# Kernel optimization log

Hardware: AMD Instinct MI355X
Metric: run time of the kernel (lower is better)

The kernel has to match this reference:

```python
import jax, jax.numpy as jnp
import numpy as np

D_MODEL, D_K, D_V, N_HEADS = 1024, 64, 64, 16
B, S = 4, 4096
LN_EPS = 1e-5
NORM_EPS = 1e-12  # torch F.normalize default eps


def setup_inputs() -> dict:
    key = jax.random.key(0)
    ks = jax.random.split(key, 9)
    s = 0.02
    return {
        "x": jax.random.normal(ks[0], (B, S, D_MODEL), dtype=jnp.float32),
        # nn.Linear weights have shape [out, in]
        "W_Q": jax.random.normal(ks[1], (N_HEADS * D_K, D_MODEL), dtype=jnp.float32) * s,
        "W_K": jax.random.normal(ks[2], (N_HEADS * D_K, D_MODEL), dtype=jnp.float32) * s,
        "W_V": jax.random.normal(ks[3], (N_HEADS * D_V, D_MODEL), dtype=jnp.float32) * s,
        "W_g": jax.random.normal(ks[4], (N_HEADS * D_V, D_MODEL), dtype=jnp.float32) * s,
        "W_alpha": jax.random.normal(ks[5], (N_HEADS, D_MODEL), dtype=jnp.float32) * s,
        "W_O": jax.random.normal(ks[6], (D_MODEL, N_HEADS * D_V), dtype=jnp.float32) * s,
        "ln_gamma": jnp.ones((D_MODEL,), dtype=jnp.float32),
        "ln_beta": jnp.zeros((D_MODEL,), dtype=jnp.float32),
    }


def reference(x, W_Q, W_K, W_V, W_g, W_alpha, W_O, ln_gamma, ln_beta):
    # --- input projection chain (unfused variant) ---
    Q_raw = jnp.einsum('bsd,od->bso', x, W_Q)               # [B,S,H*Dk] (unused downstream)
    K_raw = jnp.einsum('bsd,od->bso', x, W_K)               # [B,S,H*Dk]
    V = jnp.einsum('bsd,od->bso', x, W_V)                   # [B,S,H*Dv]
    g_raw = jnp.einsum('bsd,od->bso', x, W_g)               # [B,S,H*Dv]
    alpha_raw = jnp.einsum('bsd,od->bso', x, W_alpha)       # [B,S,H]

    # F.normalize over the full last dim (n_heads*d_k), eps clamp on the norm
    K_norm = K_raw / jnp.maximum(jnp.linalg.norm(K_raw, axis=-1, keepdims=True), NORM_EPS)
    gate = jax.nn.silu(g_raw)
    alpha = jax.nn.sigmoid(alpha_raw)

    # scan is simulated as identity: scan_output = V
    scan_output = V

    # --- output epilogue: gate-multiply + output GEMM + residual + LayerNorm ---
    gated = scan_output * gate
    projected = jnp.einsum('bsv,dv->bsd', gated, W_O)
    pre = projected + x
    mean = jnp.mean(pre, axis=-1, keepdims=True)
    var = jnp.mean(jnp.square(pre - mean), axis=-1, keepdims=True)
    out = (pre - mean) * jax.lax.rsqrt(var + LN_EPS) * ln_gamma + ln_beta
    return out
```

## Files before the change

### kernel.cpp

```cpp
#include <hip/hip_runtime.h>

#define M_TOT 16384
#define DM    1024
#define KTILES 32

typedef unsigned short ushort_t;
typedef __bf16 bf16x8 __attribute__((ext_vector_type(8)));
typedef float  f32x4  __attribute__((ext_vector_type(4)));

__device__ __forceinline__ ushort_t f32_to_bf16(float f) {
    union { float f; unsigned u; } v; v.f = f;
    unsigned u = v.u;
    return (ushort_t)((u + 0x7fffu + ((u >> 16) & 1u)) >> 16);
}
__device__ __forceinline__ float bf16_to_f32(ushort_t h) {
    union { unsigned u; float f; } v; v.u = ((unsigned)h) << 16;
    return v.f;
}

__device__ __forceinline__ int sw_off(int c) {
    return ((c >> 2) << 5) + ((((c & 3) ^ ((c >> 3) & 3))) << 3);
}

__global__ __launch_bounds__(256) void cvt_all(const float* __restrict__ x,
                                               const float* __restrict__ wv,
                                               const float* __restrict__ wg,
                                               const float* __restrict__ wo,
                                               ushort_t* __restrict__ xb,
                                               ushort_t* __restrict__ wvb,
                                               ushort_t* __restrict__ wgb,
                                               ushort_t* __restrict__ wob) {
    const long NX = (long)M_TOT * DM / 4, NW = (long)DM * DM / 4;
    long i = (long)blockIdx.x * 256 + threadIdx.x;
    const float* src; ushort_t* dst; long off;
    if (i < NX)               { src = x;  dst = xb;  off = i; }
    else if (i < NX + NW)     { src = wv; dst = wvb; off = i - NX; }
    else if (i < NX + 2 * NW) { src = wg; dst = wgb; off = i - NX - NW; }
    else                      { src = wo; dst = wob; off = i - NX - 2 * NW; }
    const float4 v = ((const float4*)src)[off];
    ushort4 o;
    o.x = f32_to_bf16(v.x); o.y = f32_to_bf16(v.y);
    o.z = f32_to_bf16(v.z); o.w = f32_to_bf16(v.w);
    ((ushort4*)dst)[off] = o;
}

__global__ __launch_bounds__(256, 3) void gemm_vg(
    const ushort_t* __restrict__ A,
    const ushort_t* __restrict__ Wv,
    const ushort_t* __restrict__ Wg,
    ushort_t* __restrict__ gated)
{
    __shared__ __align__(16) ushort_t As[2 * 4096];
    __shared__ __align__(16) ushort_t Bvs[2 * 2048];
    __shared__ __align__(16) ushort_t Bgs[2 * 2048];

    const int flat = blockIdx.x;
    const int g   = flat & 7;
    const int t   = flat >> 3;
    const int n0  = (t & 15) * 64;
    const int m0  = (((t >> 4) << 3) | g) * 128;

    const int tid  = threadIdx.x;
    const int wave = tid >> 6;
    const int lane = tid & 63;

    f32x4 accv[4][2], accg[4][2];
    const f32x4 vzero = {0.f, 0.f, 0.f, 0.f};
#pragma unroll
    for (int i = 0; i < 4; ++i)
#pragma unroll
        for (int j = 0; j < 2; ++j) { accv[i][j] = vzero; accg[i][j] = vzero; }

    const int cA0 = wave * 128 + lane, cA1 = cA0 + 64;
    const int cB  = wave * 64 + lane;
    const long gA0 = (long)(m0 + (cA0 >> 2)) * DM + ((cA0 & 3) << 3);
    const long gA1 = (long)(m0 + (cA1 >> 2)) * DM + ((cA1 & 3) << 3);
    const long gB  = (long)(n0 + (cB  >> 2)) * DM + ((cB  & 3) << 3);
    const int wA0 = sw_off(cA0), wA1 = sw_off(cA1), wB = sw_off(cB);

    const int fr   = lane & 15;
    const int quad = lane >> 4;
    const int sw   = ((quad ^ ((fr >> 1) & 3)) << 3);
    const int wmBase = (wave >> 1) * 64;
    const int wnBase = (wave & 1) * 32;
    int rdA[4], rdB[2];
#pragma unroll
    for (int i = 0; i < 4; ++i) rdA[i] = (wmBase + i * 16 + fr) * 32 + sw;
#pragma unroll
    for (int j = 0; j < 2; ++j) rdB[j] = (wnBase + j * 16 + fr) * 32 + sw;

    auto compute = [&](const ushort_t* pa, const ushort_t* pv, const ushort_t* pg) {
        bf16x8 af[4];
#pragma unroll
        for (int i = 0; i < 4; ++i) af[i] = *(const bf16x8*)(pa + rdA[i]);
#pragma unroll
        for (int j = 0; j < 2; ++j) {
            bf16x8 bv = *(const bf16x8*)(pv + rdB[j]);
            bf16x8 bg = *(const bf16x8*)(pg + rdB[j]);
#pragma unroll
            for (int i = 0; i < 4; ++i) {
                accv[i][j] = __builtin_amdgcn_mfma_f32_16x16x32_bf16(af[i], bv, accv[i][j], 0, 0, 0);
                accg[i][j] = __builtin_amdgcn_mfma_f32_16x16x32_bf16(af[i], bg, accg[i][j], 0, 0, 0);
            }
        }
    };

    int4 rA0 = *(const int4*)(A + gA0);
    int4 rA1 = *(const int4*)(A + gA1);
    int4 rV  = *(const int4*)(Wv + gB);
    int4 rG  = *(const int4*)(Wg + gB);
    unsigned xa = 0, xb = 0;
    *(int4*)(As + xa + wA0)  = rA0;
    *(int4*)(As + xa + wA1)  = rA1;
    *(int4*)(Bvs + xb + wB)  = rV;
    *(int4*)(Bgs + xb + wB)  = rG;
    __syncthreads();

    for (int kt = 0; kt < KTILES - 1; ++kt) {
        const int k0 = (kt + 1) * 32;
        rA0 = *(const int4*)(A + gA0 + k0);
        rA1 = *(const int4*)(A + gA1 + k0);
        rV  = *(const int4*)(Wv + gB + k0);
        rG  = *(const int4*)(Wg + gB + k0);
        compute(As + xa, Bvs + xb, Bgs + xb);
        xa ^= 4096; xb ^= 2048;
        *(int4*)(As + xa + wA0)  = rA0;
        *(int4*)(As + xa + wA1)  = rA1;
        *(int4*)(Bvs + xb + wB)  = rV;
        *(int4*)(Bgs + xb + wB)  = rG;
        __syncthreads();
    }
    compute(As + xa, Bvs + xb, Bgs + xb);

#pragma unroll
    for (int i = 0; i < 4; ++i) {
#pragma unroll
        for (int j = 0; j < 2; ++j) {
            const int colg = n0 + wnBase + j * 16 + fr;
#pragma unroll
            for (int r = 0; r < 4; ++r) {
                const int rowg = m0 + wmBase + i * 16 + quad * 4 + r;
                float v = accv[i][j][r];
                float gg = accg[i][j][r];
                float gate = gg / (1.0f + __expf(-gg));
                gated[rowg * DM + colg] = f32_to_bf16(v * gate);
            }
        }
    }
}

__global__ __launch_bounds__(256, 3) void gemm_o(
    const ushort_t* __restrict__ A,
    const ushort_t* __restrict__ Wo,
    const ushort_t* __restrict__ Xb,
    ushort_t* __restrict__ preout)
{
    __shared__ __align__(16) ushort_t As[2 * 4096];
    __shared__ __align__(16) ushort_t Bs[2 * 4096];

    const int flat = blockIdx.x;
    const int g   = flat & 7;
    const int t   = flat >> 3;
    const int n0  = (t & 7) * 128;
    const int m0  = (((t >> 3) << 3) | g) * 128;

    const int tid  = threadIdx.x;
    const int wave = tid >> 6;
    const int lane = tid & 63;

    f32x4 acc[4][4];
    const f32x4 vzero = {0.f, 0.f, 0.f, 0.f};
#pragma unroll
    for (int i = 0; i < 4; ++i)
#pragma unroll
        for (int j = 0; j < 4; ++j) acc[i][j] = vzero;

    const int cA0 = wave * 128 + lane, cA1 = cA0 + 64;
    const long gA0 = (long)(m0 + (cA0 >> 2)) * DM + ((cA0 & 3) << 3);
    const long gA1 = (long)(m0 + (cA1 >> 2)) * DM + ((cA1 & 3) << 3);
    const long gB0 = (long)(n0 + (cA0 >> 2)) * DM + ((cA0 & 3) << 3);
    const long gB1 = (long)(n0 + (cA1 >> 2)) * DM + ((cA1 & 3) << 3);
    const int wA0 = sw_off(cA0), wA1 = sw_off(cA1);

    const int fr   = lane & 15;
    const int quad = lane >> 4;
    const int sw   = ((quad ^ ((fr >> 1) & 3)) << 3);
    const int wmBase = (wave >> 1) * 64;
    const int wnBase = (wave & 1) * 64;
    int rdA[4], rdB[4];
#pragma unroll
    for (int i = 0; i < 4; ++i) rdA[i] = (wmBase + i * 16 + fr) * 32 + sw;
#pragma unroll
    for (int j = 0; j < 4; ++j) rdB[j] = (wnBase + j * 16 + fr) * 32 + sw;

    auto compute = [&](const ushort_t* pa, const ushort_t* pb) {
        bf16x8 af[4];
#pragma unroll
        for (int i = 0; i < 4; ++i) af[i] = *(const bf16x8*)(pa + rdA[i]);
#pragma unroll
        for (int j = 0; j < 4; ++j) {
            bf16x8 bw = *(const bf16x8*)(pb + rdB[j]);
#pragma unroll
            for (int i = 0; i < 4; ++i)
                acc[i][j] = __builtin_amdgcn_mfma_f32_16x16x32_bf16(af[i], bw, acc[i][j], 0, 0, 0);
        }
    };

    int4 rA0 = *(const int4*)(A + gA0);
    int4 rA1 = *(const int4*)(A + gA1);
    int4 rB0 = *(const int4*)(Wo + gB0);
    int4 rB1 = *(const int4*)(Wo + gB1);
    unsigned xa = 0;
    *(int4*)(As + xa + wA0) = rA0;
    *(int4*)(As + xa + wA1) = rA1;
    *(int4*)(Bs + xa + wA0) = rB0;
    *(int4*)(Bs + xa + wA1) = rB1;
    __syncthreads();

    for (int kt = 0; kt < KTILES - 1; ++kt) {
        const int k0 = (kt + 1) * 32;
        rA0 = *(const int4*)(A + gA0 + k0);
        rA1 = *(const int4*)(A + gA1 + k0);
        rB0 = *(const int4*)(Wo + gB0 + k0);
        rB1 = *(const int4*)(Wo + gB1 + k0);
        compute(As + xa, Bs + xa);
        xa ^= 4096;
        *(int4*)(As + xa + wA0) = rA0;
        *(int4*)(As + xa + wA1) = rA1;
        *(int4*)(Bs + xa + wA0) = rB0;
        *(int4*)(Bs + xa + wA1) = rB1;
        __syncthreads();
    }
    compute(As + xa, Bs + xa);

#pragma unroll
    for (int i = 0; i < 4; ++i) {
#pragma unroll
        for (int j = 0; j < 4; ++j) {
            const int colg = n0 + wnBase + j * 16 + fr;
#pragma unroll
            for (int r = 0; r < 4; ++r) {
                const int rowg = m0 + wmBase + i * 16 + quad * 4 + r;
                float pre = acc[i][j][r] + bf16_to_f32(Xb[rowg * DM + colg]);
                preout[rowg * DM + colg] = f32_to_bf16(pre);
            }
        }
    }
}

__global__ __launch_bounds__(256) void ln_rows(const ushort_t* __restrict__ pre,
                                               const float* __restrict__ gamma,
                                               const float* __restrict__ beta,
                                               float* __restrict__ out)
{
    const int row = blockIdx.x;
    const int tid = threadIdx.x;
    const int wave = tid >> 6, lane = tid & 63;

    ushort4 u = ((const ushort4*)(pre + row * DM))[tid];
    float p0 = bf16_to_f32(u.x), p1 = bf16_to_f32(u.y);
    float p2 = bf16_to_f32(u.z), p3 = bf16_to_f32(u.w);

    float s  = p0 + p1 + p2 + p3;
    float ss = p0 * p0 + p1 * p1 + p2 * p2 + p3 * p3;
#pragma unroll
    for (int off = 32; off > 0; off >>= 1) {
        s  += __shfl_down(s, off);
        ss += __shfl_down(ss, off);
    }
    __shared__ float red[8];
    __shared__ float mb[2];
    if (lane == 0) { red[wave] = s; red[4 + wave] = ss; }
    __syncthreads();
    if (tid == 0) {
        float S  = red[0] + red[1] + red[2] + red[3];
        float SS = red[4] + red[5] + red[6] + red[7];
        float mean = S * (1.0f / 1024.0f);
        float var  = SS * (1.0f / 1024.0f) - mean * mean;
        mb[0] = mean;
        mb[1] = rsqrtf(var + 1e-5f);
    }
    __syncthreads();
    const float mean = mb[0], rs = mb[1];

    float4 gm = ((const float4*)gamma)[tid];
    float4 bt = ((const float4*)beta)[tid];
    float4 o;
    o.x = (p0 - mean) * rs * gm.x + bt.x;
    o.y = (p1 - mean) * rs * gm.y + bt.y;
    o.z = (p2 - mean) * rs * gm.z + bt.z;
    o.w = (p3 - mean) * rs * gm.w + bt.w;
    ((float4*)(out + row * DM))[tid] = o;
}

extern "C" void kernel_launch(void* const* d_in, const int* in_sizes, int n_in,
                              void* d_out, int out_size, void* d_ws, size_t ws_size,
                              hipStream_t stream) {
    const float* x     = (const float*)d_in[0];
    const float* WV    = (const float*)d_in[3];
    const float* WG    = (const float*)d_in[4];
    const float* WO    = (const float*)d_in[6];
    const float* gamma = (const float*)d_in[7];
    const float* beta  = (const float*)d_in[8];
    float* out = (float*)d_out;

    char* ws = (char*)d_ws;
    ushort_t* xb    = (ushort_t*)ws;
    ushort_t* gated = (ushort_t*)(ws + (size_t)M_TOT * DM * 2);
    ushort_t* wvb   = (ushort_t*)(ws + (size_t)M_TOT * DM * 4);
    ushort_t* wgb   = (ushort_t*)(ws + (size_t)M_TOT * DM * 4 + (size_t)DM * DM * 2);
    ushort_t* wob   = (ushort_t*)(ws + (size_t)M_TOT * DM * 4 + (size_t)DM * DM * 4);
    ushort_t* pre   = xb;

    const int nCvt = (M_TOT * DM + 3 * DM * DM) / 4 / 256;
    cvt_all<<<nCvt, 256, 0, stream>>>(x, WV, WG, WO, xb, wvb, wgb, wob);

    gemm_vg<<<2048, 256, 0, stream>>>(xb, wvb, wgb, gated);
    gemm_o <<<1024, 256, 0, stream>>>(gated, wob, xb, pre);
    ln_rows<<<M_TOT, 256, 0, stream>>>(pre, gamma, beta, out);
}
```

Baseline: 284.3 us.

## Replace both GEMMs with 256x256-tile direct-to-LDS pipelined bf16 MFMA kernel

Both bf16 projection GEMMs now use one templated kernel. It has 512 threads and 256x256 output tiles, and loads global memory straight into LDS with global_load_lds, laid out in MFMA fragment order. Loads run through a 4-stage k-pipeline controlled by explicit vmcnt waits and raw barriers, and MFMA issue priority is raised. W_V and W_g are interleaved into one concatenated weight matrix in 16-row groups during conversion, so a single GEMM produces V and gate columns side by side for the SiLU-gate epilogue. The aim is more operand reuse per LDS byte and fewer register-staged copies. The cost is 128KB of dynamic LDS per block, which limits occupancy to one block per CU.

Result: faster. 273.9 us (-3.7%).

```diff
diff --git a/kernel.cpp b/kernel.cpp
--- a/kernel.cpp
+++ b/kernel.cpp
@@ -2,7 +2,6 @@
 
 #define M_TOT 16384
 #define DM    1024
-#define KTILES 32
 
 typedef unsigned short ushort_t;
 typedef __bf16 bf16x8 __attribute__((ext_vector_type(8)));
@@ -18,8 +17,11 @@
     return v.f;
 }
 
-__device__ __forceinline__ int sw_off(int c) {
-    return ((c >> 2) << 5) + ((((c & 3) ^ ((c >> 3) & 3))) << 3);
+__device__ __forceinline__ void gload16(const ushort_t* g, ushort_t* l) {
+    __builtin_amdgcn_global_load_lds(
+        (const __attribute__((address_space(1))) unsigned int*)g,
+        (__attribute__((address_space(3))) unsigned int*)l,
+        16, 0, 0);
 }
 
 __global__ __launch_bounds__(256) void cvt_all(const float* __restrict__ x,
@@ -27,224 +29,147 @@
                                                const float* __restrict__ wg,
                                                const float* __restrict__ wo,
                                                ushort_t* __restrict__ xb,
-                                               ushort_t* __restrict__ wvb,
-                                               ushort_t* __restrict__ wgb,
+                                               ushort_t* __restrict__ wcat,
                                                ushort_t* __restrict__ wob) {
     const long NX = (long)M_TOT * DM / 4, NW = (long)DM * DM / 4;
     long i = (long)blockIdx.x * 256 + threadIdx.x;
-    const float* src; ushort_t* dst; long off;
-    if (i < NX)               { src = x;  dst = xb;  off = i; }
-    else if (i < NX + NW)     { src = wv; dst = wvb; off = i - NX; }
-    else if (i < NX + 2 * NW) { src = wg; dst = wgb; off = i - NX - NW; }
-    else                      { src = wo; dst = wob; off = i - NX - 2 * NW; }
-    const float4 v = ((const float4*)src)[off];
+    const float* src; ushort_t* dst; long so, di;
+    if (i < NX) {
+        src = x; so = i; dst = xb; di = i;
+    } else if (i < NX + NW) {
+        long j = i - NX; src = wv; so = j;
+        int row = (int)(j >> 8), c4 = (int)(j & 255);
+        int orow = ((row >> 4) << 5) | (row & 15);
+        dst = wcat; di = (long)orow * 256 + c4;
+    } else if (i < NX + 2 * NW) {
+        long j = i - NX - 2 * NW + NW;
+        j = i - NX - NW; src = wg; so = j;
+        int row = (int)(j >> 8), c4 = (int)(j & 255);
+        int orow = ((row >> 4) << 5) | 16 | (row & 15);
+        dst = wcat; di = (long)orow * 256 + c4;
+    } else {
+        long j = i - NX - 2 * NW; src = wo; so = j; dst = wob; di = j;
+    }
+    const float4 v = ((const float4*)src)[so];
     ushort4 o;
     o.x = f32_to_bf16(v.x); o.y = f32_to_bf16(v.y);
     o.z = f32_to_bf16(v.z); o.w = f32_to_bf16(v.w);
-    ((ushort4*)dst)[off] = o;
-}
-
-__global__ __launch_bounds__(256, 3) void gemm_vg(
+    ((ushort4*)dst)[di] = o;
+}
+
+template<int EPI>
+__global__ __launch_bounds__(512, 2) void gemm8p(
     const ushort_t* __restrict__ A,
-    const ushort_t* __restrict__ Wv,
-    const ushort_t* __restrict__ Wg,
-    ushort_t* __restrict__ gated)
+    const ushort_t* __restrict__ B,
+    const ushort_t* __restrict__ Xb,
+    ushort_t* __restrict__ out,
+    int nchunk)
 {
-    __shared__ __align__(16) ushort_t As[2 * 4096];
-    __shared__ __align__(16) ushort_t Bvs[2 * 2048];
-    __shared__ __align__(16) ushort_t Bgs[2 * 2048];
+    extern __shared__ ushort_t lds[];
 
     const int flat = blockIdx.x;
-    const int g   = flat & 7;
-    const int t   = flat >> 3;
-    const int n0  = (t & 15) * 64;
-    const int m0  = (((t >> 4) << 3) | g) * 128;
+    const int wgid = (flat & 7) * nchunk + (flat >> 3);
+    const int m0 = (wgid & 63) << 8;
+    const int n0 = (wgid >> 6) << 8;
 
     const int tid  = threadIdx.x;
-    const int wave = tid >> 6;
-    const int lane = tid & 63;
-
-    f32x4 accv[4][2], accg[4][2];
+    const int w    = tid >> 6;
+    const int l    = tid & 63;
+    const int wm   = w >> 2;
+    const int wn   = w & 3;
+    const int fr   = l & 15;
+    const int quad = l >> 4;
+
+    f32x4 acc[8][4];
     const f32x4 vzero = {0.f, 0.f, 0.f, 0.f};
 #pragma unroll
-    for (int i = 0; i < 4; ++i)
-#pragma unroll
-        for (int j = 0; j < 2; ++j) { accv[i][j] = vzero; accg[i][j] = vzero; }
-
-    const int cA0 = wave * 128 + lane, cA1 = cA0 + 64;
-    const int cB  = wave * 64 + lane;
-    const long gA0 = (long)(m0 + (cA0 >> 2)) * DM + ((cA0 & 3) << 3);
-    const long gA1 = (long)(m0 + (cA1 >> 2)) * DM + ((cA1 & 3) << 3);
-    const long gB  = (long)(n0 + (cB  >> 2)) * DM + ((cB  & 3) << 3);
-    const int wA0 = sw_off(cA0), wA1 = sw_off(cA1), wB = sw_off(cB);
-
-    const int fr   = lane & 15;
-    const int quad = lane >> 4;
-    const int sw   = ((quad ^ ((fr >> 1) & 3)) << 3);
-    const int wmBase = (wave >> 1) * 64;
-    const int wnBase = (wave & 1) * 32;
-    int rdA[4], rdB[2];
-#pragma unroll
-    for (int i = 0; i < 4; ++i) rdA[i] = (wmBase + i * 16 + fr) * 32 + sw;
-#pragma unroll
-    for (int j = 0; j < 2; ++j) rdB[j] = (wnBase + j * 16 + fr) * 32 + sw;
-
-    auto compute = [&](const ushort_t* pa, const ushort_t* pv, const ushort_t* pg) {
-        bf16x8 af[4];
-#pragma unroll
-        for (int i = 0; i < 4; ++i) af[i] = *(const bf16x8*)(pa + rdA[i]);
-#pragma unroll
-        for (int j = 0; j < 2; ++j) {
-            bf16x8 bv = *(const bf16x8*)(pv + rdB[j]);
-            bf16x8 bg = *(const bf16x8*)(pg + rdB[j]);
-#pragma unroll
-            for (int i = 0; i < 4; ++i) {
-                accv[i][j] = __builtin_amdgcn_mfma_f32_16x16x32_bf16(af[i], bv, accv[i][j], 0, 0, 0);
-                accg[i][j] = __builtin_amdgcn_mfma_f32_16x16x32_bf16(af[i], bg, accg[i][j], 0, 0, 0);
-            }
+    for (int i = 0; i < 8; ++i)
+#pragma unroll
+        for (int j = 0; j < 4; ++j) acc[i][j] = vzero;
+
+    int srcA[2], srcB[2];
+#pragma unroll
+    for (int h = 0; h < 2; ++h) {
+        srcA[h] = (m0 + h * 128 + w * 16 + fr) * DM + (quad << 3);
+        srcB[h] = (n0 + h * 128 + w * 16 + fr) * DM + (quad << 3);
+    }
+
+    auto stage = [&](int u2) {
+        const int cS   = u2 & 1;
+        const int bufS = (u2 >> 1) & 1;
+        const int koff = (u2 >> 1) * 64 + cS * 32;
+        const int dA   = bufS * 16384 + (cS * 8 + w) * 512;
+#pragma unroll
+        for (int h = 0; h < 2; ++h) {
+            gload16(A + srcA[h] + koff, lds + dA + h * 8192);
+            gload16(B + srcB[h] + koff, lds + 32768 + dA + h * 8192);
         }
     };
 
-    int4 rA0 = *(const int4*)(A + gA0);
-    int4 rA1 = *(const int4*)(A + gA1);
-    int4 rV  = *(const int4*)(Wv + gB);
-    int4 rG  = *(const int4*)(Wg + gB);
-    unsigned xa = 0, xb = 0;
-    *(int4*)(As + xa + wA0)  = rA0;
-    *(int4*)(As + xa + wA1)  = rA1;
-    *(int4*)(Bvs + xb + wB)  = rV;
-    *(int4*)(Bgs + xb + wB)  = rG;
-    __syncthreads();
-
-    for (int kt = 0; kt < KTILES - 1; ++kt) {
-        const int k0 = (kt + 1) * 32;
-        rA0 = *(const int4*)(A + gA0 + k0);
-        rA1 = *(const int4*)(A + gA1 + k0);
-        rV  = *(const int4*)(Wv + gB + k0);
-        rG  = *(const int4*)(Wg + gB + k0);
-        compute(As + xa, Bvs + xb, Bgs + xb);
-        xa ^= 4096; xb ^= 2048;
-        *(int4*)(As + xa + wA0)  = rA0;
-        *(int4*)(As + xa + wA1)  = rA1;
-        *(int4*)(Bvs + xb + wB)  = rV;
-        *(int4*)(Bgs + xb + wB)  = rG;
-        __syncthreads();
-    }
-    compute(As + xa, Bvs + xb, Bgs + xb);
-
-#pragma unroll
-    for (int i = 0; i < 4; ++i) {
-#pragma unroll
-        for (int j = 0; j < 2; ++j) {
-            const int colg = n0 + wnBase + j * 16 + fr;
-#pragma unroll
-            for (int r = 0; r < 4; ++r) {
-                const int rowg = m0 + wmBase + i * 16 + quad * 4 + r;
-                float v = accv[i][j][r];
-                float gg = accg[i][j][r];
-                float gate = gg / (1.0f + __expf(-gg));
-                gated[rowg * DM + colg] = f32_to_bf16(v * gate);
+    stage(0); stage(1);
+
+    for (int u = 0; u < 32; ++u) {
+        if (u < 30) {
+            stage(u + 2);
+            asm volatile("s_waitcnt vmcnt(8)" ::: "memory");
+        } else if (u == 30) {
+            asm volatile("s_waitcnt vmcnt(4)" ::: "memory");
+        } else {
+            asm volatile("s_waitcnt vmcnt(0)" ::: "memory");
+        }
+        __builtin_amdgcn_s_barrier();
+
+        const int buf = (u >> 1) & 1, c = u & 1;
+        const int abase = buf * 16384 + wm * 8192 + c * 4096 + l * 8;
+        const int bbase = 32768 + buf * 16384 + (wn >> 1) * 8192
+                        + (c * 8 + (wn & 1) * 4) * 512 + l * 8;
+        bf16x8 bfrag[4], afrag[8];
+#pragma unroll
+        for (int j = 0; j < 4; ++j) bfrag[j] = *(const bf16x8*)(lds + bbase + j * 512);
+#pragma unroll
+        for (int i = 0; i < 8; ++i) afrag[i] = *(const bf16x8*)(lds + abase + i * 512);
+
+        __builtin_amdgcn_s_setprio(1);
+#pragma unroll
+        for (int j = 0; j < 4; ++j)
+#pragma unroll
+            for (int i = 0; i < 8; ++i)
+                acc[i][j] = __builtin_amdgcn_mfma_f32_16x16x32_bf16(
+                    afrag[i], bfrag[j], acc[i][j], 0, 0, 0);
+        __builtin_amdgcn_s_setprio(0);
+    }
+
+    const int rowb = m0 + wm * 128;
+    const int colb = n0 + wn * 64;
+    if (EPI == 0) {
+#pragma unroll
+        for (int i = 0; i < 8; ++i)
+#pragma unroll
+            for (int jp = 0; jp < 2; ++jp) {
+                const int cb   = colb + jp * 32;
+                const int vcol = ((cb >> 5) << 4) + fr;
+#pragma unroll
+                for (int r = 0; r < 4; ++r) {
+                    const int row = rowb + i * 16 + quad * 4 + r;
+                    float v = acc[i][2 * jp][r];
+                    float g = acc[i][2 * jp + 1][r];
+                    float gate = g / (1.0f + __expf(-g));
+                    out[row * DM + vcol] = f32_to_bf16(v * gate);
+                }
             }
-        }
-    }
-}
-
-__global__ __launch_bounds__(256, 3) void gemm_o(
-    const ushort_t* __restrict__ A,
-    const ushort_t* __restrict__ Wo,
-    const ushort_t* __restrict__ Xb,
-    ushort_t* __restrict__ preout)
-{
-    __shared__ __align__(16) ushort_t As[2 * 4096];
-    __shared__ __align__(16) ushort_t Bs[2 * 4096];
-
-    const int flat = blockIdx.x;
-    const int g   = flat & 7;
-    const int t   = flat >> 3;
-    const int n0  = (t & 7) * 128;
-    const int m0  = (((t >> 3) << 3) | g) * 128;
-
-    const int tid  = threadIdx.x;
-    const int wave = tid >> 6;
-    const int lane = tid & 63;
-
-    f32x4 acc[4][4];
-    const f32x4 vzero = {0.f, 0.f, 0.f, 0.f};
-#pragma unroll
-    for (int i = 0; i < 4; ++i)
-#pragma unroll
-        for (int j = 0; j < 4; ++j) acc[i][j] = vzero;
-
-    const int cA0 = wave * 128 + lane, cA1 = cA0 + 64;
-    const long gA0 = (long)(m0 + (cA0 >> 2)) * DM + ((cA0 & 3) << 3);
-    const long gA1 = (long)(m0 + (cA1 >> 2)) * DM + ((cA1 & 3) << 3);
-    const long gB0 = (long)(n0 + (cA0 >> 2)) * DM + ((cA0 & 3) << 3);
-    const long gB1 = (long)(n0 + (cA1 >> 2)) * DM + ((cA1 & 3) << 3);
-    const int wA0 = sw_off(cA0), wA1 = sw_off(cA1);
-
-    const int fr   = lane & 15;
-    const int quad = lane >> 4;
-    const int sw   = ((quad ^ ((fr >> 1) & 3)) << 3);
-    const int wmBase = (wave >> 1) * 64;
-    const int wnBase = (wave & 1) * 64;
-    int rdA[4], rdB[4];
-#pragma unroll
-    for (int i = 0; i < 4; ++i) rdA[i] = (wmBase + i * 16 + fr) * 32 + sw;
-#pragma unroll
-    for (int j = 0; j < 4; ++j) rdB[j] = (wnBase + j * 16 + fr) * 32 + sw;
-
-    auto compute = [&](const ushort_t* pa, const ushort_t* pb) {
-        bf16x8 af[4];
-#pragma unroll
-        for (int i = 0; i < 4; ++i) af[i] = *(const bf16x8*)(pa + rdA[i]);
-#pragma unroll
-        for (int j = 0; j < 4; ++j) {
-            bf16x8 bw = *(const bf16x8*)(pb + rdB[j]);
-#pragma unroll
-            for (int i = 0; i < 4; ++i)
-                acc[i][j] = __builtin_amdgcn_mfma_f32_16x16x32_bf16(af[i], bw, acc[i][j], 0, 0, 0);
-        }
-    };
-
-    int4 rA0 = *(const int4*)(A + gA0);
-    int4 rA1 = *(const int4*)(A + gA1);
-    int4 rB0 = *(const int4*)(Wo + gB0);
-    int4 rB1 = *(const int4*)(Wo + gB1);
-    unsigned xa = 0;
-    *(int4*)(As + xa + wA0) = rA0;
-    *(int4*)(As + xa + wA1) = rA1;
-    *(int4*)(Bs + xa + wA0) = rB0;
-    *(int4*)(Bs + xa + wA1) = rB1;
-    __syncthreads();
-
-    for (int kt = 0; kt < KTILES - 1; ++kt) {
-        const int k0 = (kt + 1) * 32;
-        rA0 = *(const int4*)(A + gA0 + k0);
-        rA1 = *(const int4*)(A + gA1 + k0);
-        rB0 = *(const int4*)(Wo + gB0 + k0);
-        rB1 = *(const int4*)(Wo + gB1 + k0);
-        compute(As + xa, Bs + xa);
-        xa ^= 4096;
-        *(int4*)(As + xa + wA0) = rA0;
-        *(int4*)(As + xa + wA1) = rA1;
-        *(int4*)(Bs + xa + wA0) = rB0;
-        *(int4*)(Bs + xa + wA1) = rB1;
-        __syncthreads();
-    }
-    compute(As + xa, Bs + xa);
-
-#pragma unroll
-    for (int i = 0; i < 4; ++i) {
-#pragma unroll
-        for (int j = 0; j < 4; ++j) {
-            const int colg = n0 + wnBase + j * 16 + fr;
-#pragma unroll
-            for (int r = 0; r < 4; ++r) {
-                const int rowg = m0 + wmBase + i * 16 + quad * 4 + r;
-                float pre = acc[i][j][r] + bf16_to_f32(Xb[rowg * DM + colg]);
-                preout[rowg * DM + colg] = f32_to_bf16(pre);
+    } else {
+#pragma unroll
+        for (int i = 0; i < 8; ++i)
+#pragma unroll
+            for (int j = 0; j < 4; ++j) {
+                const int col = colb + j * 16 + fr;
+#pragma unroll
+                for (int r = 0; r < 4; ++r) {
+                    const int row = rowb + i * 16 + quad * 4 + r;
+                    float pre = acc[i][j][r] + bf16_to_f32(Xb[row * DM + col]);
+                    out[row * DM + col] = f32_to_bf16(pre);
+                }
             }
-        }
     }
 }
 
@@ -307,15 +232,24 @@
     char* ws = (char*)d_ws;
     ushort_t* xb    = (ushort_t*)ws;
     ushort_t* gated = (ushort_t*)(ws + (size_t)M_TOT * DM * 2);
-    ushort_t* wvb   = (ushort_t*)(ws + (size_t)M_TOT * DM * 4);
-    ushort_t* wgb   = (ushort_t*)(ws + (size_t)M_TOT * DM * 4 + (size_t)DM * DM * 2);
-    ushort_t* wob   = (ushort_t*)(ws + (size_t)M_TOT * DM * 4 + (size_t)DM * DM * 4);
+    ushort_t* wcat  = (ushort_t*)(ws + (size_t)M_TOT * DM * 4);
+    ushort_t* wob   = (ushort_t*)(ws + (size_t)M_TOT * DM * 4 + (size_t)2 * DM * DM * 2);
     ushort_t* pre   = xb;
 
+    static bool attr_set = false;
+    if (!attr_set) {
+        hipFuncSetAttribute((const void*)&gemm8p<0>,
+                            hipFuncAttributeMaxDynamicSharedMemorySize, 131072);
+        hipFuncSetAttribute((const void*)&gemm8p<1>,
+                            hipFuncAttributeMaxDynamicSharedMemorySize, 131072);
+        attr_set = true;
+    }
+
     const int nCvt = (M_TOT * DM + 3 * DM * DM) / 4 / 256;
-    cvt_all<<<nCvt, 256, 0, stream>>>(x, WV, WG, WO, xb, wvb, wgb, wob);
-
-    gemm_vg<<<2048, 256, 0, stream>>>(xb, wvb, wgb, gated);
-    gemm_o <<<1024, 256, 0, stream>>>(gated, wob, xb, pre);
+    cvt_all<<<nCvt, 256, 0, stream>>>(x, WV, WG, WO, xb, wcat, wob);
+
+    gemm8p<0><<<512, 512, 131072, stream>>>(xb, wcat, nullptr, gated, 64);
+    gemm8p<1><<<256, 512, 131072, stream>>>(gated, wob, xb, pre, 32);
+
     ln_rows<<<M_TOT, 256, 0, stream>>>(pre, gamma, beta, out);
 }
```
